# Kernel optimization log

Hardware: AMD Instinct MI355X
Metric: run time of the kernel (lower is better)

## Reference

```python
import jax, jax.numpy as jnp
import numpy as np

D_MODEL = 512
DK = 4
DV = 8
HIDD = 10
HEAD = D_MODEL // DV  # 64
LN_EPS = 1e-5


def setup_inputs() -> dict:
    key = jax.random.key(0)
    ks = jax.random.split(key, 10)
    B, S, Se = 8, 512, 512
    u = jax.random.uniform  # torch.rand initializer for attention weights
    n = jax.random.normal
    return {
        "x": n(ks[0], (B, S, D_MODEL), jnp.float32),
        "x_enc": n(ks[1], (B, Se, D_MODEL), jnp.float32),
        "WqM": u(ks[2], (D_MODEL, HEAD * DK), jnp.float32),
        "WkM": u(ks[3], (D_MODEL, HEAD * DK), jnp.float32),
        "WvM": u(ks[4], (D_MODEL, HEAD * DV), jnp.float32),
        "ln_g": jnp.ones((D_MODEL,), jnp.float32),
        "ln_b": jnp.zeros((D_MODEL,), jnp.float32),
        "fc1_w": n(ks[5], (HIDD, D_MODEL), jnp.float32) * (1.0 / np.sqrt(D_MODEL)),
        "fc1_b": jnp.zeros((HIDD,), jnp.float32),
        "fc2_w": n(ks[6], (D_MODEL, HIDD), jnp.float32) * (1.0 / np.sqrt(HIDD)),
        "fc2_b": jnp.zeros((D_MODEL,), jnp.float32),
    }


def _attention(Xq, Xkv, WqM, WkM, WvM, causal_mul_mask):
    # NOTE: cross-attention in the source also uses WqM/WkM/WvM (Wq/Wk/Wv unused).
    B, Sq, _ = Xq.shape
    Sk = Xkv.shape[1]
    Q = (Xq @ WqM).reshape(B, Sq, HEAD, DK)
    K = (Xkv @ WkM).reshape(B, Sk, HEAD, DK)
    V = (Xkv @ WvM).reshape(B, Sk, HEAD, DV)
    score = jnp.einsum('bqhd,bkhd->bhqk', Q, K) / np.sqrt(DK).astype(np.float32)
    if causal_mul_mask:
        # Faithful quirk: multiplicative tril mask on scores (NOT additive -inf).
        score = score * jnp.tril(jnp.ones((Sq, Sk), score.dtype))
    w = jax.nn.softmax(score, axis=-1)
    out = jnp.einsum('bhqk,bkhd->bqhd', w, V)
    return out.reshape(B, Sq, HEAD * DV)  # HEAD*DV == d_model


def _layernorm(x, g, b):
    mu = jnp.mean(x, axis=-1, keepdims=True)
    var = jnp.mean(jnp.square(x - mu), axis=-1, keepdims=True)
    return (x - mu) * jax.lax.rsqrt(var + LN_EPS) * g + b


def reference(x, x_enc, WqM, WkM, WvM, ln_g, ln_b, fc1_w, fc1_b, fc2_w, fc2_b):
    fx = _attention(x, x, WqM, WkM, WvM, causal_mul_mask=True)
    fx = _attention(fx, x_enc, WqM, WkM, WvM, causal_mul_mask=False)
    y = _layernorm(x + fx, ln_g, ln_b)
    h = jax.nn.relu(y @ fc1_w.T + fc1_b)
    return h @ fc2_w.T + fc2_b
```

## Files before the change

kernel.cpp:

```cpp
#include <hip/hip_runtime.h>
#include <math.h>

#define D_MODEL 512
#define BATCH 8
#define SEQ 512
#define HEAD 64
#define DK 4
#define DV 8
#define HIDD 10

#define MR 32
#define KC 32
#define NC 256

__device__ __forceinline__ float4 fma4(float s, float4 w, float4 a) {
    a.x = fmaf(s, w.x, a.x); a.y = fmaf(s, w.y, a.y);
    a.z = fmaf(s, w.z, a.z); a.w = fmaf(s, w.w, a.w);
    return a;
}

__global__ __launch_bounds__(256) void proj_kernel(
    const float* __restrict__ x, const float* __restrict__ xe,
    const float* __restrict__ Wq, const float* __restrict__ Wk,
    const float* __restrict__ Wv,
    float* __restrict__ Q2, float* __restrict__ K2, float* __restrict__ V2,
    float* __restrict__ Kc, float* __restrict__ Vc)
{
    __shared__ float xt[KC * MR];
    __shared__ float wt[KC * NC];

    const int t  = threadIdx.x;
    const int bj = blockIdx.x >> 7;
    const int br = blockIdx.x & 127;
    const int r0 = br * MR;

    const float* X; const float* W; int ldw; int c0; float* dst; int vt;
    switch (bj) {
      case 0:  X = x;  W = Wq; ldw = 256; c0 = 0;   dst = Q2; vt = 0; break;
      case 1:  X = x;  W = Wk; ldw = 256; c0 = 0;   dst = K2; vt = 0; break;
      case 2:  X = x;  W = Wv; ldw = 512; c0 = 0;   dst = V2; vt = 1; break;
      case 3:  X = x;  W = Wv; ldw = 512; c0 = 256; dst = V2; vt = 1; break;
      case 4:  X = xe; W = Wk; ldw = 256; c0 = 0;   dst = Kc; vt = 0; break;
      case 5:  X = xe; W = Wv; ldw = 512; c0 = 0;   dst = Vc; vt = 1; break;
      default: X = xe; W = Wv; ldw = 512; c0 = 256; dst = Vc; vt = 1; break;
    }

    const int rg = t >> 6;
    const int cq = t & 63;
    const int rs = t & 31;
    const int kq = t >> 5;

    float4 acc[8];
#pragma unroll
    for (int r = 0; r < 8; ++r) acc[r] = make_float4(0.f, 0.f, 0.f, 0.f);

    for (int kc = 0; kc < D_MODEL; kc += KC) {
        const float4 xa = *(const float4*)(X + (long)(r0 + rs) * D_MODEL + kc + kq * 4);
        xt[(kq * 4 + 0) * MR + rs] = xa.x;
        xt[(kq * 4 + 1) * MR + rs] = xa.y;
        xt[(kq * 4 + 2) * MR + rs] = xa.z;
        xt[(kq * 4 + 3) * MR + rs] = xa.w;

#pragma unroll
        for (int i = 0; i < 8; ++i) {
            const int row = i * 4 + rg;
            *(float4*)(wt + row * NC + cq * 4) =
                *(const float4*)(W + (long)(kc + row) * ldw + c0 + cq * 4);
        }
        __syncthreads();

#pragma unroll 4
        for (int k = 0; k < KC; ++k) {
            const float4 w4 = *(const float4*)(wt + k * NC + cq * 4);
            const float4 x0 = *(const float4*)(xt + k * MR + rg * 8);
            const float4 x1 = *(const float4*)(xt + k * MR + rg * 8 + 4);
            acc[0] = fma4(x0.x, w4, acc[0]);
            acc[1] = fma4(x0.y, w4, acc[1]);
            acc[2] = fma4(x0.z, w4, acc[2]);
            acc[3] = fma4(x0.w, w4, acc[3]);
            acc[4] = fma4(x1.x, w4, acc[4]);
            acc[5] = fma4(x1.y, w4, acc[5]);
            acc[6] = fma4(x1.z, w4, acc[6]);
            acc[7] = fma4(x1.w, w4, acc[7]);
        }
        __syncthreads();
    }

    const int b = r0 >> 9;
    const int sb = (r0 & 511) + rg * 8;
    if (vt == 0) {
#pragma unroll
        for (int r = 0; r < 8; ++r)
            *(float4*)(dst + (((long)b * HEAD + cq) * SEQ + sb + r) * 4) = acc[r];
    } else {
        const int col = c0 + cq * 4;
        const int h = col >> 3;
        const int off = col & 7;
#pragma unroll
        for (int r = 0; r < 8; ++r)
            *(float4*)(dst + (((long)b * HEAD + h) * SEQ + sb + r) * 8 + off) = acc[r];
    }
}

__global__ __launch_bounds__(256, 8) void proj2_kernel(
    const float* __restrict__ A, const float* __restrict__ Wq,
    float* __restrict__ Qa, float* __restrict__ Qb)
{
    __shared__ float xt[KC * 32];
    __shared__ float wt[KC * 64];

    const int t  = threadIdx.x;
    const int kh = blockIdx.x & 1;
    const int bj = (blockIdx.x >> 1) & 3;
    const int br = blockIdx.x >> 3;
    const int r0 = br * 32;
    const int c0 = bj * 64;
    const int kb = kh * 256;
    float* dst = kh ? Qb : Qa;

    const int cq = t & 15;
    const int rr = t >> 4;
    const int rs = t & 31, kq = t >> 5;

    float4 acc[2];
    acc[0] = make_float4(0.f, 0.f, 0.f, 0.f);
    acc[1] = acc[0];

    for (int kc = 0; kc < 256; kc += KC) {
        const float4 xa = *(const float4*)(A + (long)(r0 + rs) * D_MODEL + kb + kc + kq * 4);
        xt[(kq * 4 + 0) * 32 + rs] = xa.x;
        xt[(kq * 4 + 1) * 32 + rs] = xa.y;
        xt[(kq * 4 + 2) * 32 + rs] = xa.z;
        xt[(kq * 4 + 3) * 32 + rs] = xa.w;
#pragma unroll
        for (int i = 0; i < 2; ++i) {
            const int row = i * 16 + (t >> 4);
            *(float4*)(wt + row * 64 + (t & 15) * 4) =
                *(const float4*)(Wq + (long)(kb + kc + row) * 256 + c0 + (t & 15) * 4);
        }
        __syncthreads();
#pragma unroll 4
        for (int k = 0; k < KC; ++k) {
            const float4 w4 = *(const float4*)(wt + k * 64 + cq * 4);
            const float2 x2 = *(const float2*)(xt + k * 32 + rr * 2);
            acc[0] = fma4(x2.x, w4, acc[0]);
            acc[1] = fma4(x2.y, w4, acc[1]);
        }
        __syncthreads();
    }

    const int b  = r0 >> 9;
    const int sb = (r0 & 511) + rr * 2;
    const int h  = (c0 >> 2) + cq;
#pragma unroll
    for (int r = 0; r < 2; ++r)
        *(float4*)(dst + (((long)b * HEAD + h) * SEQ + sb + r) * 4) = acc[r];
}

__global__ __launch_bounds__(256) void attn_kernel(
    const float* __restrict__ Qa, const float* __restrict__ Qb,
    const float* __restrict__ K2, const float* __restrict__ V2,
    float* __restrict__ O, int causal)
{
    extern __shared__ float smem[];
    float* Kl = smem;
    float* Vl = smem + SEQ * DK;
    float* cs = Vl + SEQ * DV;

    const int t = threadIdx.x;
    const int bh = blockIdx.x >> 1;
    const int qhalf = blockIdx.x & 1;
    const int b = bh >> 6;
    const int h = bh & 63;

    const float4* Ks = (const float4*)(K2 + (long)bh * SEQ * DK);
    ((float4*)Kl)[t]       = Ks[t];
    ((float4*)Kl)[t + 256] = Ks[t + 256];
    const float4* Vs = (const float4*)(V2 + (long)bh * SEQ * DV);
#pragma unroll
    for (int i = 0; i < 4; ++i)
        ((float4*)Vl)[t + i * 256] = Vs[t + i * 256];
    __syncthreads();

    if (causal) {
        const int ch = t >> 3, d = t & 7;
        float s16 = 0.f;
#pragma unroll
        for (int i = 0; i < 16; ++i) s16 += Vl[(ch * 16 + i) * 8 + d];
        cs[ch * 8 + d] = s16;
        __syncthreads();
        if (t < 8) {
            cs[256 + t] = 0.f;
            float run = 0.f;
            for (int c2 = 31; c2 >= 0; --c2) {
                run += cs[c2 * 8 + t];
                cs[c2 * 8 + t] = run;
            }
        }
        __syncthreads();
    }

    const int q = qhalf * 256 + t;
    float4 qv = *(const float4*)(Qa + ((long)bh * SEQ + q) * 4);
    if (Qb) {
        const float4 qw = *(const float4*)(Qb + ((long)bh * SEQ + q) * 4);
        qv.x += qw.x; qv.y += qw.y; qv.z += qw.z; qv.w += qw.w;
    }
    const float cf = 0.5f * 1.44269504088896340736f;
    const float q0 = qv.x * cf, q1 = qv.y * cf;
    const float q2 = qv.z * cf, q3 = qv.w * cf;

    const int bound = causal ? q : (SEQ - 1);

    float m = -INFINITY, l = 0.f;
    float a0=0.f,a1=0.f,a2=0.f,a3=0.f,a4=0.f,a5=0.f,a6=0.f,a7=0.f;

    int s0 = 0;
    for (; s0 + 8 <= bound + 1; s0 += 8) {
        float sc[8];
#pragma unroll
        for (int i = 0; i < 8; ++i) {
            const float4 k4 = *(const float4*)(Kl + (s0 + i) * 4);
            sc[i] = fmaf(q0, k4.x, fmaf(q1, k4.y, fmaf(q2, k4.z, q3 * k4.w)));
        }
        float gm = fmaxf(fmaxf(fmaxf(sc[0], sc[1]), fmaxf(sc[2], sc[3])),
                         fmaxf(fmaxf(sc[4], sc[5]), fmaxf(sc[6], sc[7])));
        if (gm > m) {
            float scale = __builtin_amdgcn_exp2f(m - gm);
            l *= scale;
            a0*=scale; a1*=scale; a2*=scale; a3*=scale;
            a4*=scale; a5*=scale; a6*=scale; a7*=scale;
            m = gm;
        }
#pragma unroll
        for (int i = 0; i < 8; ++i) {
            float p = __builtin_amdgcn_exp2f(sc[i] - m);
            l += p;
            const float4 v0 = *(const float4*)(Vl + (s0 + i) * 8);
            const float4 v1 = *(const float4*)(Vl + (s0 + i) * 8 + 4);
            a0 = fmaf(p, v0.x, a0); a1 = fmaf(p, v0.y, a1);
            a2 = fmaf(p, v0.z, a2); a3 = fmaf(p, v0.w, a3);
            a4 = fmaf(p, v1.x, a4); a5 = fmaf(p, v1.y, a5);
            a6 = fmaf(p, v1.z, a6); a7 = fmaf(p, v1.w, a7);
        }
    }
    for (int s = s0; s <= bound; ++s) {
        const float4 k4 = *(const float4*)(Kl + s * 4);
        float sc = fmaf(q0, k4.x, fmaf(q1, k4.y, fmaf(q2, k4.z, q3 * k4.w)));
        if (sc > m) {
            float scale = __builtin_amdgcn_exp2f(m - sc);
            l *= scale;
            a0*=scale; a1*=scale; a2*=scale; a3*=scale;
            a4*=scale; a5*=scale; a6*=scale; a7*=scale;
            m = sc;
        }
        float p = __builtin_amdgcn_exp2f(sc - m);
        l += p;
        const float4 v0 = *(const float4*)(Vl + s * 8);
        const float4 v1 = *(const float4*)(Vl + s * 8 + 4);
        a0 = fmaf(p, v0.x, a0); a1 = fmaf(p, v0.y, a1);
        a2 = fmaf(p, v0.z, a2); a3 = fmaf(p, v0.w, a3);
        a4 = fmaf(p, v1.x, a4); a5 = fmaf(p, v1.y, a5);
        a6 = fmaf(p, v1.z, a6); a7 = fmaf(p, v1.w, a7);
    }

    if (causal && q < SEQ - 1) {
        float M = fmaxf(m, 0.f);
        float scale = __builtin_amdgcn_exp2f(m - M);
        float pm = __builtin_amdgcn_exp2f(-M);
        l = l * scale + pm * (float)(SEQ - 1 - q);
        int nq = q + 1;
        int cq2 = nq >> 4;
        float sv[8];
#pragma unroll
        for (int d = 0; d < 8; ++d) sv[d] = cs[(cq2 + 1) * 8 + d];
        for (int s = nq; s < (cq2 + 1) * 16; ++s) {
            const float4 v0 = *(const float4*)(Vl + s * 8);
            const float4 v1 = *(const float4*)(Vl + s * 8 + 4);
            sv[0]+=v0.x; sv[1]+=v0.y; sv[2]+=v0.z; sv[3]+=v0.w;
            sv[4]+=v1.x; sv[5]+=v1.y; sv[6]+=v1.z; sv[7]+=v1.w;
        }
        a0 = a0*scale + pm*sv[0]; a1 = a1*scale + pm*sv[1];
        a2 = a2*scale + pm*sv[2]; a3 = a3*scale + pm*sv[3];
        a4 = a4*scale + pm*sv[4]; a5 = a5*scale + pm*sv[5];
        a6 = a6*scale + pm*sv[6]; a7 = a7*scale + pm*sv[7];
    }

    float inv = 1.0f / l;
    const long obase = (long)b * SEQ * 512 + (long)q * 512 + h * DV;
    *(float4*)(O + obase)     = make_float4(a0*inv, a1*inv, a2*inv, a3*inv);
    *(float4*)(O + obase + 4) = make_float4(a4*inv, a5*inv, a6*inv, a7*inv);
}

__global__ __launch_bounds__(256) void ln_mlp_kernel(
    const float* __restrict__ x, const float* __restrict__ fx,
    const float* __restrict__ g, const float* __restrict__ beta,
    const float* __restrict__ w1, const float* __restrict__ b1,
    const float* __restrict__ w2, const float* __restrict__ b2,
    float* __restrict__ out)
{
    const int t = threadIdx.x;
    const int lane = t & 63;
    const int row = blockIdx.x * 4 + (t >> 6);
    const long base = (long)row * D_MODEL;
    const int e0 = lane * 8;

    const float4 xa = *(const float4*)(x + base + e0);
    const float4 xb = *(const float4*)(x + base + e0 + 4);
    const float4 fa = *(const float4*)(fx + base + e0);
    const float4 fb = *(const float4*)(fx + base + e0 + 4);
    float z[8] = {xa.x+fa.x, xa.y+fa.y, xa.z+fa.z, xa.w+fa.w,
                  xb.x+fb.x, xb.y+fb.y, xb.z+fb.z, xb.w+fb.w};

    float sum = 0.f;
#pragma unroll
    for (int j = 0; j < 8; ++j) sum += z[j];
#pragma unroll
    for (int o = 32; o > 0; o >>= 1) sum += __shfl_xor(sum, o);
    float mu = sum * (1.0f / 512.0f);

    float d[8], ss = 0.f;
#pragma unroll
    for (int j = 0; j < 8; ++j) { d[j] = z[j] - mu; ss += d[j] * d[j]; }
#pragma unroll
    for (int o = 32; o > 0; o >>= 1) ss += __shfl_xor(ss, o);
    float rs = rsqrtf(ss * (1.0f / 512.0f) + 1e-5f);

    const float4 ga = *(const float4*)(g + e0);
    const float4 gb = *(const float4*)(g + e0 + 4);
    const float4 ba = *(const float4*)(beta + e0);
    const float4 bb = *(const float4*)(beta + e0 + 4);
    const float gg[8] = {ga.x,ga.y,ga.z,ga.w,gb.x,gb.y,gb.z,gb.w};
    const float bt[8] = {ba.x,ba.y,ba.z,ba.w,bb.x,bb.y,bb.z,bb.w};
    float y[8];
#pragma unroll
    for (int j = 0; j < 8; ++j) y[j] = d[j] * rs * gg[j] + bt[j];

    float part[HIDD];
#pragma unroll
    for (int i = 0; i < HIDD; ++i) {
        const float4 wa = *(const float4*)(w1 + i * 512 + e0);
        const float4 wb = *(const float4*)(w1 + i * 512 + e0 + 4);
        part[i] = y[0]*wa.x + y[1]*wa.y + y[2]*wa.z + y[3]*wa.w
                + y[4]*wb.x + y[5]*wb.y + y[6]*wb.z + y[7]*wb.w;
    }
#pragma unroll
    for (int i = 0; i < HIDD; ++i)
#pragma unroll
        for (int o = 32; o > 0; o >>= 1) part[i] += __shfl_xor(part[i], o);

    float hv[HIDD];
#pragma unroll
    for (int i = 0; i < HIDD; ++i) hv[i] = fmaxf(part[i] + b1[i], 0.f);

    float o8[8];
#pragma unroll
    for (int j = 0; j < 8; ++j) o8[j] = b2[e0 + j];
#pragma unroll
    for (int i = 0; i < HIDD; ++i)
#pragma unroll
        for (int j = 0; j < 8; ++j)
            o8[j] = fmaf(hv[i], w2[(long)(e0 + j) * 10 + i], o8[j]);

    *(float4*)(out + base + e0)     = make_float4(o8[0], o8[1], o8[2], o8[3]);
    *(float4*)(out + base + e0 + 4) = make_float4(o8[4], o8[5], o8[6], o8[7]);
}

extern "C" void kernel_launch(void* const* d_in, const int* in_sizes, int n_in,
                              void* d_out, int out_size, void* d_ws, size_t ws_size,
                              hipStream_t stream) {
    (void)in_sizes; (void)n_in; (void)out_size; (void)ws_size;
    const float* x    = (const float*)d_in[0];
    const float* xenc = (const float*)d_in[1];
    const float* Wq   = (const float*)d_in[2];
    const float* Wk   = (const float*)d_in[3];
    const float* Wv   = (const float*)d_in[4];
    const float* ln_g = (const float*)d_in[5];
    const float* ln_b = (const float*)d_in[6];
    const float* w1   = (const float*)d_in[7];
    const float* b1   = (const float*)d_in[8];
    const float* w2   = (const float*)d_in[9];
    const float* b2   = (const float*)d_in[10];
    float* out = (float*)d_out;

    float* ws = (float*)d_ws;
    float* Q1 = ws;
    float* K1 = ws +  1048576;
    float* V1 = ws +  2097152;
    float* Kc = ws +  4194304;
    float* Vc = ws +  5242880;
    float* A  = ws +  7340032;
    float* Qa = ws +  9437184;
    float* Qb = ws + 10485760;

    const size_t lds_cross  = (size_t)(SEQ * DK + SEQ * DV) * 4;
    const size_t lds_causal = lds_cross + (size_t)(33 * DV) * 4;

    proj_kernel<<<dim3(896), 256, 0, stream>>>(x, xenc, Wq, Wk, Wv,
                                               Q1, K1, V1, Kc, Vc);
    attn_kernel<<<dim3(BATCH * HEAD * 2), 256, lds_causal, stream>>>(
        Q1, nullptr, K1, V1, A, 1);
    proj2_kernel<<<dim3(1024), 256, 0, stream>>>(A, Wq, Qa, Qb);
    attn_kernel<<<dim3(BATCH * HEAD * 2), 256, lds_cross, stream>>>(
        Qa, Qb, Kc, Vc, A, 0);
    ln_mlp_kernel<<<dim3(1024), 256, 0, stream>>>(x, A, ln_g, ln_b,
                                                  w1, b1, w2, b2, out);
}
```

Baseline: 343.3 us.

## Retile projection GEMM to 64x128 tiles with single-wave blocks and block swizzle

The input projection kernel now uses 64-thread blocks, each computing a 64x128 output tile with a 16x8 register micro-tile per thread, instead of 256-thread blocks computing 32x256 tiles. The aim is more FMA work per shared-memory load and less LDS traffic per flop. A block-index swizzle spreads neighbouring blocks across row tiles to improve cache sharing of X and W. The trade-off is higher register pressure (128 accumulators) and fewer threads per block, which may reduce latency hiding.

```diff
diff --git a/kernel.cpp b/kernel.cpp
--- a/kernel.cpp
+++ b/kernel.cpp
@@ -9,9 +9,9 @@
 #define DV 8
 #define HIDD 10
 
-#define MR 32
-#define KC 32
-#define NC 256
+#define PMR 64
+#define PNC 128
+#define PKC 32
 
 __device__ __forceinline__ float4 fma4(float s, float4 w, float4 a) {
     a.x = fmaf(s, w.x, a.x); a.y = fmaf(s, w.y, a.y);
@@ -19,86 +19,107 @@
     return a;
 }
 
-__global__ __launch_bounds__(256) void proj_kernel(
+__global__ __launch_bounds__(64, 2) void proj_kernel(
     const float* __restrict__ x, const float* __restrict__ xe,
     const float* __restrict__ Wq, const float* __restrict__ Wk,
     const float* __restrict__ Wv,
     float* __restrict__ Q2, float* __restrict__ K2, float* __restrict__ V2,
     float* __restrict__ Kc, float* __restrict__ Vc)
 {
-    __shared__ float xt[KC * MR];
-    __shared__ float wt[KC * NC];
-
-    const int t  = threadIdx.x;
-    const int bj = blockIdx.x >> 7;
-    const int br = blockIdx.x & 127;
-    const int r0 = br * MR;
+    __shared__ float xt[PKC][PMR];
+    __shared__ float wt[PKC][PNC];
+
+    const int t = threadIdx.x;
+    const int swz = (blockIdx.x & 7) * 112 + (blockIdx.x >> 3);
+    const int bj = swz % 14;
+    const int br = swz / 14;
+    const int r0 = br * PMR;
 
     const float* X; const float* W; int ldw; int c0; float* dst; int vt;
-    switch (bj) {
-      case 0:  X = x;  W = Wq; ldw = 256; c0 = 0;   dst = Q2; vt = 0; break;
-      case 1:  X = x;  W = Wk; ldw = 256; c0 = 0;   dst = K2; vt = 0; break;
-      case 2:  X = x;  W = Wv; ldw = 512; c0 = 0;   dst = V2; vt = 1; break;
-      case 3:  X = x;  W = Wv; ldw = 512; c0 = 256; dst = V2; vt = 1; break;
-      case 4:  X = xe; W = Wk; ldw = 256; c0 = 0;   dst = Kc; vt = 0; break;
-      case 5:  X = xe; W = Wv; ldw = 512; c0 = 0;   dst = Vc; vt = 1; break;
-      default: X = xe; W = Wv; ldw = 512; c0 = 256; dst = Vc; vt = 1; break;
-    }
-
-    const int rg = t >> 6;
-    const int cq = t & 63;
-    const int rs = t & 31;
-    const int kq = t >> 5;
-
-    float4 acc[8];
-#pragma unroll
-    for (int r = 0; r < 8; ++r) acc[r] = make_float4(0.f, 0.f, 0.f, 0.f);
-
-    for (int kc = 0; kc < D_MODEL; kc += KC) {
-        const float4 xa = *(const float4*)(X + (long)(r0 + rs) * D_MODEL + kc + kq * 4);
-        xt[(kq * 4 + 0) * MR + rs] = xa.x;
-        xt[(kq * 4 + 1) * MR + rs] = xa.y;
-        xt[(kq * 4 + 2) * MR + rs] = xa.z;
-        xt[(kq * 4 + 3) * MR + rs] = xa.w;
-
-#pragma unroll
-        for (int i = 0; i < 8; ++i) {
-            const int row = i * 4 + rg;
-            *(float4*)(wt + row * NC + cq * 4) =
-                *(const float4*)(W + (long)(kc + row) * ldw + c0 + cq * 4);
-        }
-        __syncthreads();
-
-#pragma unroll 4
-        for (int k = 0; k < KC; ++k) {
-            const float4 w4 = *(const float4*)(wt + k * NC + cq * 4);
-            const float4 x0 = *(const float4*)(xt + k * MR + rg * 8);
-            const float4 x1 = *(const float4*)(xt + k * MR + rg * 8 + 4);
-            acc[0] = fma4(x0.x, w4, acc[0]);
-            acc[1] = fma4(x0.y, w4, acc[1]);
-            acc[2] = fma4(x0.z, w4, acc[2]);
-            acc[3] = fma4(x0.w, w4, acc[3]);
-            acc[4] = fma4(x1.x, w4, acc[4]);
-            acc[5] = fma4(x1.y, w4, acc[5]);
-            acc[6] = fma4(x1.z, w4, acc[6]);
-            acc[7] = fma4(x1.w, w4, acc[7]);
+    if (bj < 2)       { X = x;  W = Wq; ldw = 256; c0 = bj * 128;         dst = Q2; vt = 0; }
+    else if (bj < 4)  { X = x;  W = Wk; ldw = 256; c0 = (bj - 2) * 128;   dst = K2; vt = 0; }
+    else if (bj < 8)  { X = x;  W = Wv; ldw = 512; c0 = (bj - 4) * 128;   dst = V2; vt = 1; }
+    else if (bj < 10) { X = xe; W = Wk; ldw = 256; c0 = (bj - 8) * 128;   dst = Kc; vt = 0; }
+    else              { X = xe; W = Wv; ldw = 512; c0 = (bj - 10) * 128;  dst = Vc; vt = 1; }
+
+    const int rg = t >> 4;
+    const int cq = t & 15;
+
+    float4 acc[16][2];
+#pragma unroll
+    for (int r = 0; r < 16; ++r) {
+        acc[r][0] = make_float4(0.f, 0.f, 0.f, 0.f);
+        acc[r][1] = make_float4(0.f, 0.f, 0.f, 0.f);
+    }
+
+    for (int kc = 0; kc < D_MODEL; kc += PKC) {
+        {
+            const float* xr = X + (long)(r0 + t) * D_MODEL + kc;
+#pragma unroll
+            for (int i = 0; i < 8; ++i) {
+                const float4 v = *(const float4*)(xr + i * 4);
+                xt[i * 4 + 0][t] = v.x;
+                xt[i * 4 + 1][t] = v.y;
+                xt[i * 4 + 2][t] = v.z;
+                xt[i * 4 + 3][t] = v.w;
+            }
+        }
+        {
+            const int cw = (t & 31) * 4;
+            const int k0 = t >> 5;
+#pragma unroll
+            for (int i = 0; i < 16; ++i) {
+                const int kr = k0 + i * 2;
+                *(float4*)(&wt[kr][cw]) =
+                    *(const float4*)(W + (long)(kc + kr) * ldw + c0 + cw);
+            }
+        }
+        __syncthreads();
+
+#pragma unroll 2
+        for (int k = 0; k < PKC; ++k) {
+            const float4 x0 = *(const float4*)(&xt[k][rg * 16 + 0]);
+            const float4 x1 = *(const float4*)(&xt[k][rg * 16 + 4]);
+            const float4 x2 = *(const float4*)(&xt[k][rg * 16 + 8]);
+            const float4 x3 = *(const float4*)(&xt[k][rg * 16 + 12]);
+            const float4 w0 = *(const float4*)(&wt[k][cq * 4]);
+            const float4 w1 = *(const float4*)(&wt[k][64 + cq * 4]);
+            const float xv[16] = {x0.x, x0.y, x0.z, x0.w,
+                                  x1.x, x1.y, x1.z, x1.w,
+                                  x2.x, x2.y, x2.z, x2.w,
+                                  x3.x, x3.y, x3.z, x3.w};
+#pragma unroll
+            for (int r = 0; r < 16; ++r) {
+                acc[r][0] = fma4(xv[r], w0, acc[r][0]);
+                acc[r][1] = fma4(xv[r], w1, acc[r][1]);
+            }
         }
         __syncthreads();
     }
 
     const int b = r0 >> 9;
-    const int sb = (r0 & 511) + rg * 8;
     if (vt == 0) {
 #pragma unroll
-        for (int r = 0; r < 8; ++r)
-            *(float4*)(dst + (((long)b * HEAD + cq) * SEQ + sb + r) * 4) = acc[r];
+        for (int ci = 0; ci < 2; ++ci) {
+            const int h = (c0 >> 2) + ci * 16 + cq;
+#pragma unroll
+            for (int r = 0; r < 16; ++r) {
+                const int s = (r0 & 511) + rg * 16 + r;
+                *(float4*)(dst + (((long)b * HEAD + h) * SEQ + s) * 4) = acc[r][ci];
+            }
+        }
     } else {
-        const int col = c0 + cq * 4;
-        const int h = col >> 3;
-        const int off = col & 7;
-#pragma unroll
-        for (int r = 0; r < 8; ++r)
-            *(float4*)(dst + (((long)b * HEAD + h) * SEQ + sb + r) * 8 + off) = acc[r];
+#pragma unroll
+        for (int ci = 0; ci < 2; ++ci) {
+            const int c = c0 + ci * 64 + cq * 4;
+            const int h = c >> 3;
+            const int off = c & 7;
+#pragma unroll
+            for (int r = 0; r < 16; ++r) {
+                const int s = (r0 & 511) + rg * 16 + r;
+                *(float4*)(dst + (((long)b * HEAD + h) * SEQ + s) * 8 + off) = acc[r][ci];
+            }
+        }
     }
 }
 
@@ -106,8 +127,8 @@
     const float* __restrict__ A, const float* __restrict__ Wq,
     float* __restrict__ Qa, float* __restrict__ Qb)
 {
-    __shared__ float xt[KC * 32];
-    __shared__ float wt[KC * 64];
+    __shared__ float xt[32 * 32];
+    __shared__ float wt[32 * 64];
 
     const int t  = threadIdx.x;
     const int kh = blockIdx.x & 1;
@@ -126,7 +147,7 @@
     acc[0] = make_float4(0.f, 0.f, 0.f, 0.f);
     acc[1] = acc[0];
 
-    for (int kc = 0; kc < 256; kc += KC) {
+    for (int kc = 0; kc < 256; kc += 32) {
         const float4 xa = *(const float4*)(A + (long)(r0 + rs) * D_MODEL + kb + kc + kq * 4);
         xt[(kq * 4 + 0) * 32 + rs] = xa.x;
         xt[(kq * 4 + 1) * 32 + rs] = xa.y;
@@ -140,7 +161,7 @@
         }
         __syncthreads();
 #pragma unroll 4
-        for (int k = 0; k < KC; ++k) {
+        for (int k = 0; k < 32; ++k) {
             const float4 w4 = *(const float4*)(wt + k * 64 + cq * 4);
             const float2 x2 = *(const float2*)(xt + k * 32 + rr * 2);
             acc[0] = fma4(x2.x, w4, acc[0]);
@@ -396,8 +417,8 @@
     const size_t lds_cross  = (size_t)(SEQ * DK + SEQ * DV) * 4;
     const size_t lds_causal = lds_cross + (size_t)(33 * DV) * 4;
 
-    proj_kernel<<<dim3(896), 256, 0, stream>>>(x, xenc, Wq, Wk, Wv,
-                                               Q1, K1, V1, Kc, Vc);
+    proj_kernel<<<dim3(896), 64, 0, stream>>>(x, xenc, Wq, Wk, Wv,
+                                              Q1, K1, V1, Kc, Vc);
     attn_kernel<<<dim3(BATCH * HEAD * 2), 256, lds_causal, stream>>>(
         Q1, nullptr, K1, V1, A, 1);
     proj2_kernel<<<dim3(1024), 256, 0, stream>>>(A, Wq, Qa, Qb);
```

Measured after the change: 406.8 us. 1.18x slower.

## Process two queries per thread in attention and compute causal masked scores directly

Applied to the files above, without the earlier changes.

The attention kernel now runs one block per (batch, head), and each thread handles two queries, so every K/V value read from shared memory feeds two score and accumulate streams. The causal path drops the prefix-sum shortcut for masked positions. It now loops over all 512 keys and sets masked scores to zero inline, which removes divergent loop bounds and the extra syncs. The cost is that causal work roughly doubles, since the masked half is no longer closed-form. The grid is also halved, leaving fewer blocks to hide latency.

```diff
diff --git a/kernel.cpp b/kernel.cpp
--- a/kernel.cpp
+++ b/kernel.cpp
@@ -106,8 +106,8 @@
     const float* __restrict__ A, const float* __restrict__ Wq,
     float* __restrict__ Qa, float* __restrict__ Qb)
 {
-    __shared__ float xt[KC * 32];
-    __shared__ float wt[KC * 64];
+    __shared__ float xt[32 * 32];
+    __shared__ float wt[32 * 64];
 
     const int t  = threadIdx.x;
     const int kh = blockIdx.x & 1;
@@ -126,7 +126,7 @@
     acc[0] = make_float4(0.f, 0.f, 0.f, 0.f);
     acc[1] = acc[0];
 
-    for (int kc = 0; kc < 256; kc += KC) {
+    for (int kc = 0; kc < 256; kc += 32) {
         const float4 xa = *(const float4*)(A + (long)(r0 + rs) * D_MODEL + kb + kc + kq * 4);
         xt[(kq * 4 + 0) * 32 + rs] = xa.x;
         xt[(kq * 4 + 1) * 32 + rs] = xa.y;
@@ -140,7 +140,7 @@
         }
         __syncthreads();
 #pragma unroll 4
-        for (int k = 0; k < KC; ++k) {
+        for (int k = 0; k < 32; ++k) {
             const float4 w4 = *(const float4*)(wt + k * 64 + cq * 4);
             const float2 x2 = *(const float2*)(xt + k * 32 + rr * 2);
             acc[0] = fma4(x2.x, w4, acc[0]);
@@ -157,21 +157,85 @@
         *(float4*)(dst + (((long)b * HEAD + h) * SEQ + sb + r) * 4) = acc[r];
 }
 
+template <int CAUSAL>
+__device__ __forceinline__ void attn_core(
+    const float* __restrict__ Kl, const float* __restrict__ Vl,
+    const int q1, const int q2,
+    const float4 qv1, const float4 qv2,
+    float* __restrict__ O, const long obase1, const long obase2)
+{
+    float m1 = -INFINITY, l1 = 0.f, m2 = -INFINITY, l2 = 0.f;
+    float A1[8], A2[8];
+#pragma unroll
+    for (int j = 0; j < 8; ++j) { A1[j] = 0.f; A2[j] = 0.f; }
+
+    for (int s0 = 0; s0 < SEQ; s0 += 8) {
+        float sc1[8], sc2[8];
+#pragma unroll
+        for (int i = 0; i < 8; ++i) {
+            const float4 k4 = *(const float4*)(Kl + (s0 + i) * 4);
+            const float d1 = fmaf(qv1.x, k4.x, fmaf(qv1.y, k4.y,
+                             fmaf(qv1.z, k4.z, qv1.w * k4.w)));
+            const float d2 = fmaf(qv2.x, k4.x, fmaf(qv2.y, k4.y,
+                             fmaf(qv2.z, k4.z, qv2.w * k4.w)));
+            sc1[i] = (CAUSAL && (s0 + i) > q1) ? 0.f : d1;
+            sc2[i] = (CAUSAL && (s0 + i) > q2) ? 0.f : d2;
+        }
+        const float g1 = fmaxf(fmaxf(fmaxf(sc1[0], sc1[1]), fmaxf(sc1[2], sc1[3])),
+                               fmaxf(fmaxf(sc1[4], sc1[5]), fmaxf(sc1[6], sc1[7])));
+        const float g2 = fmaxf(fmaxf(fmaxf(sc2[0], sc2[1]), fmaxf(sc2[2], sc2[3])),
+                               fmaxf(fmaxf(sc2[4], sc2[5]), fmaxf(sc2[6], sc2[7])));
+        if (g1 > m1) {
+            const float sc = __builtin_amdgcn_exp2f(m1 - g1);
+            l1 *= sc;
+#pragma unroll
+            for (int j = 0; j < 8; ++j) A1[j] *= sc;
+            m1 = g1;
+        }
+        if (g2 > m2) {
+            const float sc = __builtin_amdgcn_exp2f(m2 - g2);
+            l2 *= sc;
+#pragma unroll
+            for (int j = 0; j < 8; ++j) A2[j] *= sc;
+            m2 = g2;
+        }
+#pragma unroll
+        for (int i = 0; i < 8; ++i) {
+            const float p1 = __builtin_amdgcn_exp2f(sc1[i] - m1);
+            const float p2 = __builtin_amdgcn_exp2f(sc2[i] - m2);
+            l1 += p1; l2 += p2;
+            const float4 v0 = *(const float4*)(Vl + (s0 + i) * 8);
+            const float4 v1 = *(const float4*)(Vl + (s0 + i) * 8 + 4);
+            A1[0] = fmaf(p1, v0.x, A1[0]); A1[1] = fmaf(p1, v0.y, A1[1]);
+            A1[2] = fmaf(p1, v0.z, A1[2]); A1[3] = fmaf(p1, v0.w, A1[3]);
+            A1[4] = fmaf(p1, v1.x, A1[4]); A1[5] = fmaf(p1, v1.y, A1[5]);
+            A1[6] = fmaf(p1, v1.z, A1[6]); A1[7] = fmaf(p1, v1.w, A1[7]);
+            A2[0] = fmaf(p2, v0.x, A2[0]); A2[1] = fmaf(p2, v0.y, A2[1]);
+            A2[2] = fmaf(p2, v0.z, A2[2]); A2[3] = fmaf(p2, v0.w, A2[3]);
+            A2[4] = fmaf(p2, v1.x, A2[4]); A2[5] = fmaf(p2, v1.y, A2[5]);
+            A2[6] = fmaf(p2, v1.z, A2[6]); A2[7] = fmaf(p2, v1.w, A2[7]);
+        }
+    }
+
+    const float i1 = 1.0f / l1, i2 = 1.0f / l2;
+    *(float4*)(O + obase1)     = make_float4(A1[0]*i1, A1[1]*i1, A1[2]*i1, A1[3]*i1);
+    *(float4*)(O + obase1 + 4) = make_float4(A1[4]*i1, A1[5]*i1, A1[6]*i1, A1[7]*i1);
+    *(float4*)(O + obase2)     = make_float4(A2[0]*i2, A2[1]*i2, A2[2]*i2, A2[3]*i2);
+    *(float4*)(O + obase2 + 4) = make_float4(A2[4]*i2, A2[5]*i2, A2[6]*i2, A2[7]*i2);
+}
+
 __global__ __launch_bounds__(256) void attn_kernel(
     const float* __restrict__ Qa, const float* __restrict__ Qb,
     const float* __restrict__ K2, const float* __restrict__ V2,
     float* __restrict__ O, int causal)
 {
-    extern __shared__ float smem[];
-    float* Kl = smem;
-    float* Vl = smem + SEQ * DK;
-    float* cs = Vl + SEQ * DV;
-
-    const int t = threadIdx.x;
-    const int bh = blockIdx.x >> 1;
-    const int qhalf = blockIdx.x & 1;
-    const int b = bh >> 6;
-    const int h = bh & 63;
+    __shared__ float Kl[SEQ * DK];
+    __shared__ float Vl[SEQ * DV];
+
+    const int t  = threadIdx.x;
+    const int bh = blockIdx.x;
+    const int b  = bh >> 6;
+    const int h  = bh & 63;
 
     const float4* Ks = (const float4*)(K2 + (long)bh * SEQ * DK);
     ((float4*)Kl)[t]       = Ks[t];
@@ -180,116 +244,29 @@
 #pragma unroll
     for (int i = 0; i < 4; ++i)
         ((float4*)Vl)[t + i * 256] = Vs[t + i * 256];
+
+    const int q1 = t, q2 = t + 256;
+    float4 qv1 = *(const float4*)(Qa + ((long)bh * SEQ + q1) * 4);
+    float4 qv2 = *(const float4*)(Qa + ((long)bh * SEQ + q2) * 4);
+    if (Qb) {
+        const float4 w1 = *(const float4*)(Qb + ((long)bh * SEQ + q1) * 4);
+        const float4 w2 = *(const float4*)(Qb + ((long)bh * SEQ + q2) * 4);
+        qv1.x += w1.x; qv1.y += w1.y; qv1.z += w1.z; qv1.w += w1.w;
+        qv2.x += w2.x; qv2.y += w2.y; qv2.z += w2.z; qv2.w += w2.w;
+    }
+    const float cf = 0.5f * 1.44269504088896340736f;
+    qv1.x *= cf; qv1.y *= cf; qv1.z *= cf; qv1.w *= cf;
+    qv2.x *= cf; qv2.y *= cf; qv2.z *= cf; qv2.w *= cf;
+
     __syncthreads();
 
-    if (causal) {
-        const int ch = t >> 3, d = t & 7;
-        float s16 = 0.f;
-#pragma unroll
-        for (int i = 0; i < 16; ++i) s16 += Vl[(ch * 16 + i) * 8 + d];
-        cs[ch * 8 + d] = s16;
-        __syncthreads();
-        if (t < 8) {
-            cs[256 + t] = 0.f;
-            float run = 0.f;
-            for (int c2 = 31; c2 >= 0; --c2) {
-                run += cs[c2 * 8 + t];
-                cs[c2 * 8 + t] = run;
-            }
-        }
-        __syncthreads();
-    }
-
-    const int q = qhalf * 256 + t;
-    float4 qv = *(const float4*)(Qa + ((long)bh * SEQ + q) * 4);
-    if (Qb) {
-        const float4 qw = *(const float4*)(Qb + ((long)bh * SEQ + q) * 4);
-        qv.x += qw.x; qv.y += qw.y; qv.z += qw.z; qv.w += qw.w;
-    }
-    const float cf = 0.5f * 1.44269504088896340736f;
-    const float q0 = qv.x * cf, q1 = qv.y * cf;
-    const float q2 = qv.z * cf, q3 = qv.w * cf;
-
-    const int bound = causal ? q : (SEQ - 1);
-
-    float m = -INFINITY, l = 0.f;
-    float a0=0.f,a1=0.f,a2=0.f,a3=0.f,a4=0.f,a5=0.f,a6=0.f,a7=0.f;
-
-    int s0 = 0;
-    for (; s0 + 8 <= bound + 1; s0 += 8) {
-        float sc[8];
-#pragma unroll
-        for (int i = 0; i < 8; ++i) {
-            const float4 k4 = *(const float4*)(Kl + (s0 + i) * 4);
-            sc[i] = fmaf(q0, k4.x, fmaf(q1, k4.y, fmaf(q2, k4.z, q3 * k4.w)));
-        }
-        float gm = fmaxf(fmaxf(fmaxf(sc[0], sc[1]), fmaxf(sc[2], sc[3])),
-                         fmaxf(fmaxf(sc[4], sc[5]), fmaxf(sc[6], sc[7])));
-        if (gm > m) {
-            float scale = __builtin_amdgcn_exp2f(m - gm);
-            l *= scale;
-            a0*=scale; a1*=scale; a2*=scale; a3*=scale;
-            a4*=scale; a5*=scale; a6*=scale; a7*=scale;
-            m = gm;
-        }
-#pragma unroll
-        for (int i = 0; i < 8; ++i) {
-            float p = __builtin_amdgcn_exp2f(sc[i] - m);
-            l += p;
-            const float4 v0 = *(const float4*)(Vl + (s0 + i) * 8);
-            const float4 v1 = *(const float4*)(Vl + (s0 + i) * 8 + 4);
-            a0 = fmaf(p, v0.x, a0); a1 = fmaf(p, v0.y, a1);
-            a2 = fmaf(p, v0.z, a2); a3 = fmaf(p, v0.w, a3);
-            a4 = fmaf(p, v1.x, a4); a5 = fmaf(p, v1.y, a5);
-            a6 = fmaf(p, v1.z, a6); a7 = fmaf(p, v1.w, a7);
-        }
-    }
-    for (int s = s0; s <= bound; ++s) {
-        const float4 k4 = *(const float4*)(Kl + s * 4);
-        float sc = fmaf(q0, k4.x, fmaf(q1, k4.y, fmaf(q2, k4.z, q3 * k4.w)));
-        if (sc > m) {
-            float scale = __builtin_amdgcn_exp2f(m - sc);
-            l *= scale;
-            a0*=scale; a1*=scale; a2*=scale; a3*=scale;
-            a4*=scale; a5*=scale; a6*=scale; a7*=scale;
-            m = sc;
-        }
-        float p = __builtin_amdgcn_exp2f(sc - m);
-        l += p;
-        const float4 v0 = *(const float4*)(Vl + s * 8);
-        const float4 v1 = *(const float4*)(Vl + s * 8 + 4);
-        a0 = fmaf(p, v0.x, a0); a1 = fmaf(p, v0.y, a1);
-        a2 = fmaf(p, v0.z, a2); a3 = fmaf(p, v0.w, a3);
-        a4 = fmaf(p, v1.x, a4); a5 = fmaf(p, v1.y, a5);
-        a6 = fmaf(p, v1.z, a6); a7 = fmaf(p, v1.w, a7);
-    }
-
-    if (causal && q < SEQ - 1) {
-        float M = fmaxf(m, 0.f);
-        float scale = __builtin_amdgcn_exp2f(m - M);
-        float pm = __builtin_amdgcn_exp2f(-M);
-        l = l * scale + pm * (float)(SEQ - 1 - q);
-        int nq = q + 1;
-        int cq2 = nq >> 4;
-        float sv[8];
-#pragma unroll
-        for (int d = 0; d < 8; ++d) sv[d] = cs[(cq2 + 1) * 8 + d];
-        for (int s = nq; s < (cq2 + 1) * 16; ++s) {
-            const float4 v0 = *(const float4*)(Vl + s * 8);
-            const float4 v1 = *(const float4*)(Vl + s * 8 + 4);
-            sv[0]+=v0.x; sv[1]+=v0.y; sv[2]+=v0.z; sv[3]+=v0.w;
-            sv[4]+=v1.x; sv[5]+=v1.y; sv[6]+=v1.z; sv[7]+=v1.w;
-        }
-        a0 = a0*scale + pm*sv[0]; a1 = a1*scale + pm*sv[1];
-        a2 = a2*scale + pm*sv[2]; a3 = a3*scale + pm*sv[3];
-        a4 = a4*scale + pm*sv[4]; a5 = a5*scale + pm*sv[5];
-        a6 = a6*scale + pm*sv[6]; a7 = a7*scale + pm*sv[7];
-    }
-
-    float inv = 1.0f / l;
-    const long obase = (long)b * SEQ * 512 + (long)q * 512 + h * DV;
-    *(float4*)(O + obase)     = make_float4(a0*inv, a1*inv, a2*inv, a3*inv);
-    *(float4*)(O + obase + 4) = make_float4(a4*inv, a5*inv, a6*inv, a7*inv);
+    const long ob1 = (long)b * SEQ * 512 + (long)q1 * 512 + h * DV;
+    const long ob2 = (long)b * SEQ * 512 + (long)q2 * 512 + h * DV;
+
+    if (causal)
+        attn_core<1>(Kl, Vl, q1, q2, qv1, qv2, O, ob1, ob2);
+    else
+        attn_core<0>(Kl, Vl, q1, q2, qv1, qv2, O, ob1, ob2);
 }
 
 __global__ __launch_bounds__(256) void ln_mlp_kernel(
@@ -393,15 +370,12 @@
     float* Qa = ws +  9437184;
     float* Qb = ws + 10485760;
 
-    const size_t lds_cross  = (size_t)(SEQ * DK + SEQ * DV) * 4;
-    const size_t lds_causal = lds_cross + (size_t)(33 * DV) * 4;
-
     proj_kernel<<<dim3(896), 256, 0, stream>>>(x, xenc, Wq, Wk, Wv,
                                                Q1, K1, V1, Kc, Vc);
-    attn_kernel<<<dim3(BATCH * HEAD * 2), 256, lds_causal, stream>>>(
+    attn_kernel<<<dim3(BATCH * HEAD), 256, 0, stream>>>(
         Q1, nullptr, K1, V1, A, 1);
     proj2_kernel<<<dim3(1024), 256, 0, stream>>>(A, Wq, Qa, Qb);
-    attn_kernel<<<dim3(BATCH * HEAD * 2), 256, lds_cross, stream>>>(
+    attn_kernel<<<dim3(BATCH * HEAD), 256, 0, stream>>>(
         Qa, Qb, Kc, Vc, A, 0);
     ln_mlp_kernel<<<dim3(1024), 256, 0, stream>>>(x, A, ln_g, ln_b,
                                                   w1, b1, w2, b2, out);
```

Result: slower. 353.1 us (+2.9%).

## Pre-transpose inputs and stream X operand from global into registers in projection

Applied to the files above, without the earlier changes.

Adds a transpose kernel that writes x and x_enc in column-major form, so the projection GEMM can read its X operand directly from global memory as contiguous float4 pairs per k. The X tile is no longer staged in shared memory, and the next k's values are prefetched one step ahead in registers. The workspace is re-laid out so that A, Qa and Qb alias the transposed buffers. The cost is an extra kernel launch plus a full read and write of both inputs, and per-k global loads inside the inner loop that rely on the cache.

```diff
diff --git a/kernel.cpp b/kernel.cpp
--- a/kernel.cpp
+++ b/kernel.cpp
@@ -19,14 +19,43 @@
     return a;
 }
 
+__global__ __launch_bounds__(256) void transpose_kernel(
+    const float* __restrict__ x, const float* __restrict__ xe,
+    float* __restrict__ xT, float* __restrict__ xeT)
+{
+    __shared__ float tile[64][65];
+    int bid = blockIdx.x;
+    const float* src; float* dst;
+    if (bid < 512) { src = x;  dst = xT; }
+    else           { src = xe; dst = xeT; bid -= 512; }
+    const int R0 = (bid >> 3) * 64;
+    const int C0 = (bid & 7) * 64;
+    const int t = threadIdx.x;
+    const int rr = t >> 4, c4 = (t & 15) * 4;
+#pragma unroll
+    for (int i = 0; i < 4; ++i) {
+        const float4 v = *(const float4*)(src + (long)(R0 + i * 16 + rr) * 512 + C0 + c4);
+        tile[i * 16 + rr][c4 + 0] = v.x; tile[i * 16 + rr][c4 + 1] = v.y;
+        tile[i * 16 + rr][c4 + 2] = v.z; tile[i * 16 + rr][c4 + 3] = v.w;
+    }
+    __syncthreads();
+#pragma unroll
+    for (int i = 0; i < 4; ++i) {
+        const int oc = i * 16 + rr;
+        float4 v;
+        v.x = tile[c4 + 0][oc]; v.y = tile[c4 + 1][oc];
+        v.z = tile[c4 + 2][oc]; v.w = tile[c4 + 3][oc];
+        *(float4*)(dst + (long)(C0 + oc) * 4096 + R0 + c4) = v;
+    }
+}
+
 __global__ __launch_bounds__(256) void proj_kernel(
-    const float* __restrict__ x, const float* __restrict__ xe,
+    const float* __restrict__ xT, const float* __restrict__ xeT,
     const float* __restrict__ Wq, const float* __restrict__ Wk,
     const float* __restrict__ Wv,
     float* __restrict__ Q2, float* __restrict__ K2, float* __restrict__ V2,
     float* __restrict__ Kc, float* __restrict__ Vc)
 {
-    __shared__ float xt[KC * MR];
     __shared__ float wt[KC * NC];
 
     const int t  = threadIdx.x;
@@ -34,33 +63,29 @@
     const int br = blockIdx.x & 127;
     const int r0 = br * MR;
 
-    const float* X; const float* W; int ldw; int c0; float* dst; int vt;
+    const float* XT; const float* W; int ldw; int c0; float* dst; int vt;
     switch (bj) {
-      case 0:  X = x;  W = Wq; ldw = 256; c0 = 0;   dst = Q2; vt = 0; break;
-      case 1:  X = x;  W = Wk; ldw = 256; c0 = 0;   dst = K2; vt = 0; break;
-      case 2:  X = x;  W = Wv; ldw = 512; c0 = 0;   dst = V2; vt = 1; break;
-      case 3:  X = x;  W = Wv; ldw = 512; c0 = 256; dst = V2; vt = 1; break;
-      case 4:  X = xe; W = Wk; ldw = 256; c0 = 0;   dst = Kc; vt = 0; break;
-      case 5:  X = xe; W = Wv; ldw = 512; c0 = 0;   dst = Vc; vt = 1; break;
-      default: X = xe; W = Wv; ldw = 512; c0 = 256; dst = Vc; vt = 1; break;
+      case 0:  XT = xT;  W = Wq; ldw = 256; c0 = 0;   dst = Q2; vt = 0; break;
+      case 1:  XT = xT;  W = Wk; ldw = 256; c0 = 0;   dst = K2; vt = 0; break;
+      case 2:  XT = xT;  W = Wv; ldw = 512; c0 = 0;   dst = V2; vt = 1; break;
+      case 3:  XT = xT;  W = Wv; ldw = 512; c0 = 256; dst = V2; vt = 1; break;
+      case 4:  XT = xeT; W = Wk; ldw = 256; c0 = 0;   dst = Kc; vt = 0; break;
+      case 5:  XT = xeT; W = Wv; ldw = 512; c0 = 0;   dst = Vc; vt = 1; break;
+      default: XT = xeT; W = Wv; ldw = 512; c0 = 256; dst = Vc; vt = 1; break;
     }
 
     const int rg = t >> 6;
     const int cq = t & 63;
-    const int rs = t & 31;
-    const int kq = t >> 5;
+    const float* xp = XT + r0 + rg * 8;
 
     float4 acc[8];
 #pragma unroll
     for (int r = 0; r < 8; ++r) acc[r] = make_float4(0.f, 0.f, 0.f, 0.f);
 
+    float4 xa0 = *(const float4*)(xp);
+    float4 xa1 = *(const float4*)(xp + 4);
+
     for (int kc = 0; kc < D_MODEL; kc += KC) {
-        const float4 xa = *(const float4*)(X + (long)(r0 + rs) * D_MODEL + kc + kq * 4);
-        xt[(kq * 4 + 0) * MR + rs] = xa.x;
-        xt[(kq * 4 + 1) * MR + rs] = xa.y;
-        xt[(kq * 4 + 2) * MR + rs] = xa.z;
-        xt[(kq * 4 + 3) * MR + rs] = xa.w;
-
 #pragma unroll
         for (int i = 0; i < 8; ++i) {
             const int row = i * 4 + rg;
@@ -71,17 +96,20 @@
 
 #pragma unroll 4
         for (int k = 0; k < KC; ++k) {
+            const int kn = kc + k + 1;
+            const float* xpn = xp + (long)(kn < 512 ? kn : 511) * 4096;
+            const float4 xb0 = *(const float4*)(xpn);
+            const float4 xb1 = *(const float4*)(xpn + 4);
             const float4 w4 = *(const float4*)(wt + k * NC + cq * 4);
-            const float4 x0 = *(const float4*)(xt + k * MR + rg * 8);
-            const float4 x1 = *(const float4*)(xt + k * MR + rg * 8 + 4);
-            acc[0] = fma4(x0.x, w4, acc[0]);
-            acc[1] = fma4(x0.y, w4, acc[1]);
-            acc[2] = fma4(x0.z, w4, acc[2]);
-            acc[3] = fma4(x0.w, w4, acc[3]);
-            acc[4] = fma4(x1.x, w4, acc[4]);
-            acc[5] = fma4(x1.y, w4, acc[5]);
-            acc[6] = fma4(x1.z, w4, acc[6]);
-            acc[7] = fma4(x1.w, w4, acc[7]);
+            acc[0] = fma4(xa0.x, w4, acc[0]);
+            acc[1] = fma4(xa0.y, w4, acc[1]);
+            acc[2] = fma4(xa0.z, w4, acc[2]);
+            acc[3] = fma4(xa0.w, w4, acc[3]);
+            acc[4] = fma4(xa1.x, w4, acc[4]);
+            acc[5] = fma4(xa1.y, w4, acc[5]);
+            acc[6] = fma4(xa1.z, w4, acc[6]);
+            acc[7] = fma4(xa1.w, w4, acc[7]);
+            xa0 = xb0; xa1 = xb1;
         }
         __syncthreads();
     }
@@ -89,6 +117,10 @@
     const int b = r0 >> 9;
     const int sb = (r0 & 511) + rg * 8;
     if (vt == 0) {
+#pragma unroll
+        for (int r = 0; r < 8; ++r) {
+            (void)r;
+        }
 #pragma unroll
         for (int r = 0; r < 8; ++r)
             *(float4*)(dst + (((long)b * HEAD + cq) * SEQ + sb + r) * 4) = acc[r];
@@ -106,8 +138,8 @@
     const float* __restrict__ A, const float* __restrict__ Wq,
     float* __restrict__ Qa, float* __restrict__ Qb)
 {
-    __shared__ float xt[KC * 32];
-    __shared__ float wt[KC * 64];
+    __shared__ float xt[32 * 32];
+    __shared__ float wt[32 * 64];
 
     const int t  = threadIdx.x;
     const int kh = blockIdx.x & 1;
@@ -126,7 +158,7 @@
     acc[0] = make_float4(0.f, 0.f, 0.f, 0.f);
     acc[1] = acc[0];
 
-    for (int kc = 0; kc < 256; kc += KC) {
+    for (int kc = 0; kc < 256; kc += 32) {
         const float4 xa = *(const float4*)(A + (long)(r0 + rs) * D_MODEL + kb + kc + kq * 4);
         xt[(kq * 4 + 0) * 32 + rs] = xa.x;
         xt[(kq * 4 + 1) * 32 + rs] = xa.y;
@@ -140,7 +172,7 @@
         }
         __syncthreads();
 #pragma unroll 4
-        for (int k = 0; k < KC; ++k) {
+        for (int k = 0; k < 32; ++k) {
             const float4 w4 = *(const float4*)(wt + k * 64 + cq * 4);
             const float2 x2 = *(const float2*)(xt + k * 32 + rr * 2);
             acc[0] = fma4(x2.x, w4, acc[0]);
@@ -383,20 +415,23 @@
     const float* b2   = (const float*)d_in[10];
     float* out = (float*)d_out;
 
-    float* ws = (float*)d_ws;
-    float* Q1 = ws;
-    float* K1 = ws +  1048576;
-    float* V1 = ws +  2097152;
-    float* Kc = ws +  4194304;
-    float* Vc = ws +  5242880;
-    float* A  = ws +  7340032;
-    float* Qa = ws +  9437184;
-    float* Qb = ws + 10485760;
+    float* ws  = (float*)d_ws;
+    float* xT  = ws;
+    float* xeT = ws + 2097152;
+    float* Q1  = ws + 4194304;
+    float* K1  = ws + 5242880;
+    float* V1  = ws + 6291456;
+    float* Kc  = ws + 8388608;
+    float* Vc  = ws + 9437184;
+    float* A   = ws;
+    float* Qa  = ws + 2097152;
+    float* Qb  = ws + 3145728;
 
     const size_t lds_cross  = (size_t)(SEQ * DK + SEQ * DV) * 4;
     const size_t lds_causal = lds_cross + (size_t)(33 * DV) * 4;
 
-    proj_kernel<<<dim3(896), 256, 0, stream>>>(x, xenc, Wq, Wk, Wv,
+    transpose_kernel<<<dim3(1024), 256, 0, stream>>>(x, xenc, xT, xeT);
+    proj_kernel<<<dim3(896), 256, 0, stream>>>(xT, xeT, Wq, Wk, Wv,
                                                Q1, K1, V1, Kc, Vc);
     attn_kernel<<<dim3(BATCH * HEAD * 2), 256, lds_causal, stream>>>(
         Q1, nullptr, K1, V1, A, 1);
```

Result: slower. 383.0 us (+11.6%).
